# Kernel optimization log

Hardware: AMD Instinct MI355X
Metric: run time of the kernel (lower is better)

## Reference

```python
import jax, jax.numpy as jnp
import numpy as np

KERNEL_SIZE = 5
KERNEL_NUM = 64
STRIDE = 1
PRIOR_VAR = 1.0


def setup_inputs() -> dict:
    key = jax.random.key(0)
    k1, k2 = jax.random.split(key)
    mu_in = jax.random.normal(k1, (128, 128, 128, 3), dtype=jnp.float32)
    # init: normal stddev 0.05 for w_mu, constant -4.6 for w_sigma
    w_mu = 0.05 * jax.random.normal(k2, (KERNEL_SIZE, KERNEL_SIZE, 3, KERNEL_NUM), dtype=jnp.float32)
    w_sigma = jnp.full((KERNEL_NUM,), -4.6, dtype=jnp.float32)
    return {"mu_in": mu_in, "w_mu": w_mu, "w_sigma": w_sigma}


def kl_regularizer_conv(mu, logvar):
    k = mu.shape[-1]
    mu2 = mu.reshape(-1, k)              # [k*k*C, kernel_num]
    n = mu2.shape[0]
    kl = -jnp.mean(1.0 + logvar
                   - jnp.log1p(jnp.exp(logvar)) / PRIOR_VAR
                   - jnp.sum(jnp.square(mu2), axis=0) / (n * PRIOR_VAR))
    kl = jnp.where(jnp.isnan(kl), jnp.float32(1e-05), kl)
    kl = jnp.where(jnp.isinf(kl), jnp.float32(1e-05), kl)
    return kl


def reference(mu_in, w_mu, w_sigma):
    B, H, W, C = mu_in.shape
    ks = KERNEL_SIZE
    kl_conv = kl_regularizer_conv(w_mu, w_sigma)
    w_sigma_2 = jnp.log1p(jnp.exp(w_sigma))  # softplus

    dn = ('NHWC', 'HWIO', 'NHWC')
    mu_out = jax.lax.conv_general_dilated(
        mu_in, w_mu, window_strides=(STRIDE, STRIDE), padding='VALID',
        dimension_numbers=dn)  # [B, Ho, Wo, kernel_num]

    # Per-patch sum of squares == sum-pool conv over squared input summed over C
    # (mathematically identical to extract_patches -> square -> sum, no im2col blowup)
    sq = jnp.sum(jnp.square(mu_in), axis=-1, keepdims=True)  # [B,H,W,1]
    ones_k = jnp.ones((ks, ks, 1, 1), dtype=mu_in.dtype)
    patch_ss = jax.lax.conv_general_dilated(
        sq, ones_k, window_strides=(STRIDE, STRIDE), padding='VALID',
        dimension_numbers=dn)  # [B, Ho, Wo, 1]
    x_dim = jnp.float32(ks * ks * C)
    # broadcast: softplus(w_sigma)[kn] * (sum_sq / x_dim)[B,Ho,Wo,1]
    Sigma_out = w_sigma_2 * (patch_ss / x_dim)  # [B, Ho, Wo, kernel_num]

    Ho = mu_out.shape[1]
    Sigma_out = Sigma_out.reshape(B, Ho, Ho, KERNEL_NUM)
    return (mu_out, Sigma_out, kl_conv)
```

## Files before the change

### kernel.cpp

```cpp
#include <hip/hip_runtime.h>
#include <hip/hip_bf16.h>
#include <math.h>

#define KS 5
#define CIN 3
#define KN 64
#define HIN 128
#define HO 124
#define ROWF (HIN * CIN)
#define NOUT (128LL * 124 * 124 * 64)

typedef short bfrag8 __attribute__((ext_vector_type(8)));
typedef float ffrag4 __attribute__((ext_vector_type(4)));

__device__ __forceinline__ unsigned short f2bf(float f) {
    union { float f; unsigned u; } x;
    x.f = f;
    unsigned r = x.u + 0x7fffu + ((x.u >> 16) & 1u);
    return (unsigned short)(r >> 16);
}

__global__ void kl_kernel(const float* __restrict__ w_mu,
                          const float* __restrict__ w_sigma,
                          float* __restrict__ out_kl) {
    int kn = threadIdx.x;
    float s = 0.f;
#pragma unroll
    for (int i = 0; i < 75; ++i) {
        float m = w_mu[i * KN + kn];
        s = fmaf(m, m, s);
    }
    float lv = w_sigma[kn];
    float sp = log1pf(expf(lv));
    float val = 1.0f + lv - sp - s * (1.0f / 75.0f);
#pragma unroll
    for (int off = 32; off > 0; off >>= 1) val += __shfl_down(val, off);
    if (kn == 0) {
        float kl = -(val / 64.0f);
        if (isnan(kl) || isinf(kl)) kl = 1e-5f;
        out_kl[0] = kl;
    }
}

__global__ __launch_bounds__(256, 4) void conv_kernel(
    const float* __restrict__ mu_in,
    const float* __restrict__ w_mu,
    const float* __restrict__ w_sigma,
    float* __restrict__ mu_out,
    float* __restrict__ sig_out) {

    __shared__ __align__(16) float s_in[2336];
    __shared__ __align__(16) unsigned short s_w[64 * 104];
    __shared__ float s_sp[KN];
    __shared__ float s_cs[HIN];
    __shared__ float s_ssn[HO];

    const int bid = blockIdx.x;
    const int b = bid / HO;
    const int ho = bid % HO;
    const int tid = threadIdx.x;

    const float* src = mu_in + (size_t)(b * HIN + ho) * ROWF;
    for (int i = tid; i < 480; i += 256)
        reinterpret_cast<float4*>(s_in)[i] =
            reinterpret_cast<const float4*>(src)[i];
    for (int i = 1920 + tid; i < 2336; i += 256) s_in[i] = 0.f;

    {
        const int n = tid >> 2;
        const int kbase = (tid & 3) * 26;
#pragma unroll
        for (int kk = 0; kk < 26; ++kk) {
            const int k = kbase + kk;
            float v = 0.f;
            if (k < 80) {
                const int r = k >> 4, t = k & 15;
                if (t < 15) v = w_mu[(r * 15 + t) * KN + n];
            }
            s_w[n * 104 + k] = f2bf(v);
        }
    }
    if (tid < KN) s_sp[tid] = log1pf(expf(w_sigma[tid]));
    __syncthreads();

    if (tid < HIN) {
        float cs = 0.f;
#pragma unroll
        for (int r = 0; r < KS; ++r)
#pragma unroll
            for (int c = 0; c < CIN; ++c) {
                float v = s_in[r * ROWF + tid * CIN + c];
                cs = fmaf(v, v, cs);
            }
        s_cs[tid] = cs;
    }
    __syncthreads();
    if (tid < HO) {
        float ss = s_cs[tid] + s_cs[tid + 1] + s_cs[tid + 2] + s_cs[tid + 3] +
                   s_cs[tid + 4];
        s_ssn[tid] = ss * (1.0f / 75.0f);
    }
    __syncthreads();

    const int lane = tid & 63;
    const int wid = tid >> 6;
    const int lhi = lane >> 4;
    const int llo = lane & 15;

    ffrag4 acc[2][4];
#pragma unroll
    for (int m = 0; m < 2; ++m)
#pragma unroll
        for (int n = 0; n < 4; ++n) acc[m][n] = (ffrag4){0.f, 0.f, 0.f, 0.f};

#pragma unroll
    for (int ks = 0; ks < 3; ++ks) {
        const int k0 = ks * 32 + lhi * 8;
        bfrag8 bfr[4];
#pragma unroll
        for (int nt = 0; nt < 4; ++nt)
            bfr[nt] = *reinterpret_cast<const bfrag8*>(
                &s_w[(nt * 16 + llo) * 104 + k0]);

        const int r = k0 >> 4;
        const int off = k0 & 15;
#pragma unroll
        for (int mt = 0; mt < 2; ++mt) {
            const int wo = wid * 32 + mt * 16 + llo;
            const float* ap = &s_in[r * ROWF + wo * CIN + off];
            bfrag8 afr;
#pragma unroll
            for (int j = 0; j < 8; ++j) afr[j] = (short)f2bf(ap[j]);
#pragma unroll
            for (int nt = 0; nt < 4; ++nt)
                acc[mt][nt] = __builtin_amdgcn_mfma_f32_16x16x32_bf16(
                    afr, bfr[nt], acc[mt][nt], 0, 0, 0);
        }
    }

    float spv[4];
#pragma unroll
    for (int nt = 0; nt < 4; ++nt) spv[nt] = s_sp[nt * 16 + llo];

    const size_t orow = (size_t)(b * HO + ho) * (size_t)(HO * KN);
#pragma unroll
    for (int mt = 0; mt < 2; ++mt) {
#pragma unroll
        for (int rg = 0; rg < 4; ++rg) {
            const int wo = wid * 32 + mt * 16 + lhi * 4 + rg;
            if (wo < HO) {
                const float ssn = s_ssn[wo];
                const size_t obase = orow + (size_t)wo * KN;
#pragma unroll
                for (int nt = 0; nt < 4; ++nt) {
                    const int kn = nt * 16 + llo;
                    mu_out[obase + kn] = acc[mt][nt][rg];
                    sig_out[obase + kn] = spv[nt] * ssn;
                }
            }
        }
    }
}

extern "C" void kernel_launch(void* const* d_in, const int* in_sizes, int n_in,
                              void* d_out, int out_size, void* d_ws,
                              size_t ws_size, hipStream_t stream) {
    const float* mu_in = (const float*)d_in[0];
    const float* w_mu = (const float*)d_in[1];
    const float* w_sigma = (const float*)d_in[2];
    float* out = (float*)d_out;

    float* mu_out = out;
    float* sig_out = out + NOUT;
    float* kl_out = out + 2 * NOUT;

    conv_kernel<<<128 * HO, 256, 0, stream>>>(mu_in, w_mu, w_sigma, mu_out,
                                              sig_out);
    kl_kernel<<<1, 64, 0, stream>>>(w_mu, w_sigma, kl_out);
}
```

Baseline: 265.8 us.

## Precompute bf16 weights once, swap MFMA operands for vectorized float4 output stores

Moves the weight bf16 conversion and softplus into a one-block prep kernel that writes to workspace, so each conv block copies ready weights with vector loads. The input row is pre-converted to bf16 in shared memory once. The MFMA operand roles are swapped (weights as A, input as B) so each lane holds four consecutive output channels and can write mu_out and sig_out with float4 stores instead of scalar stores. This adds a kernel launch and more shared memory, and lowers the occupancy hint from 4 to 3 blocks per CU.

```diff
diff --git a/kernel.cpp b/kernel.cpp
--- a/kernel.cpp
+++ b/kernel.cpp
@@ -9,6 +9,7 @@
 #define HO 124
 #define ROWF (HIN * CIN)
 #define NOUT (128LL * 124 * 124 * 64)
+#define KP 104
 
 typedef short bfrag8 __attribute__((ext_vector_type(8)));
 typedef float ffrag4 __attribute__((ext_vector_type(4)));
@@ -20,6 +21,26 @@
     return (unsigned short)(r >> 16);
 }
 
+__global__ void prep_kernel(const float* __restrict__ w_mu,
+                            const float* __restrict__ w_sigma,
+                            unsigned short* __restrict__ w_bf,
+                            float* __restrict__ sp_out) {
+    const int tid = threadIdx.x;
+    const int n = tid >> 2;
+    const int kbase = (tid & 3) * 26;
+#pragma unroll
+    for (int kk = 0; kk < 26; ++kk) {
+        const int k = kbase + kk;
+        float v = 0.f;
+        if (k < 80) {
+            const int r = k >> 4, t = k & 15;
+            if (t < 15) v = w_mu[(r * 15 + t) * KN + n];
+        }
+        w_bf[n * KP + k] = f2bf(v);
+    }
+    if (tid < KN) sp_out[tid] = log1pf(expf(w_sigma[tid]));
+}
+
 __global__ void kl_kernel(const float* __restrict__ w_mu,
                           const float* __restrict__ w_sigma,
                           float* __restrict__ out_kl) {
@@ -42,18 +63,19 @@
     }
 }
 
-__global__ __launch_bounds__(256, 4) void conv_kernel(
+__global__ __launch_bounds__(256, 3) void conv_kernel(
     const float* __restrict__ mu_in,
-    const float* __restrict__ w_mu,
-    const float* __restrict__ w_sigma,
+    const unsigned short* __restrict__ w_bf,
+    const float* __restrict__ sp_in,
     float* __restrict__ mu_out,
     float* __restrict__ sig_out) {
 
-    __shared__ __align__(16) float s_in[2336];
-    __shared__ __align__(16) unsigned short s_w[64 * 104];
+    __shared__ __align__(16) float s_in[1952];
+    __shared__ __align__(16) unsigned short s_x[128 * KP];
+    __shared__ __align__(16) unsigned short s_w[KN * KP];
     __shared__ float s_sp[KN];
     __shared__ float s_cs[HIN];
-    __shared__ float s_ssn[HO];
+    __shared__ float s_ssn[HIN];
 
     const int bid = blockIdx.x;
     const int b = bid / HO;
@@ -64,23 +86,11 @@
     for (int i = tid; i < 480; i += 256)
         reinterpret_cast<float4*>(s_in)[i] =
             reinterpret_cast<const float4*>(src)[i];
-    for (int i = 1920 + tid; i < 2336; i += 256) s_in[i] = 0.f;
-
-    {
-        const int n = tid >> 2;
-        const int kbase = (tid & 3) * 26;
-#pragma unroll
-        for (int kk = 0; kk < 26; ++kk) {
-            const int k = kbase + kk;
-            float v = 0.f;
-            if (k < 80) {
-                const int r = k >> 4, t = k & 15;
-                if (t < 15) v = w_mu[(r * 15 + t) * KN + n];
-            }
-            s_w[n * 104 + k] = f2bf(v);
-        }
-    }
-    if (tid < KN) s_sp[tid] = log1pf(expf(w_sigma[tid]));
+    if (tid < 32) s_in[1920 + tid] = 0.f;
+    for (int i = tid; i < 832; i += 256)
+        reinterpret_cast<float4*>(s_w)[i] =
+            reinterpret_cast<const float4*>(w_bf)[i];
+    if (tid < KN) s_sp[tid] = sp_in[tid];
     __syncthreads();
 
     if (tid < HIN) {
@@ -95,68 +105,86 @@
         s_cs[tid] = cs;
     }
     __syncthreads();
-    if (tid < HO) {
-        float ss = s_cs[tid] + s_cs[tid + 1] + s_cs[tid + 2] + s_cs[tid + 3] +
-                   s_cs[tid + 4];
-        s_ssn[tid] = ss * (1.0f / 75.0f);
+
+    if (tid < HIN) {
+        float v = 0.f;
+        if (tid < HO)
+            v = (s_cs[tid] + s_cs[tid + 1] + s_cs[tid + 2] + s_cs[tid + 3] +
+                 s_cs[tid + 4]) * (1.0f / 75.0f);
+        s_ssn[tid] = v;
+    }
+    for (int i = tid; i < 640; i += 256) {
+        const int r = i >> 7;
+        const int wo = i & 127;
+        const float* p = &s_in[r * ROWF + wo * CIN];
+        unsigned u[8];
+#pragma unroll
+        for (int j = 0; j < 8; ++j)
+            u[j] = (unsigned)f2bf(p[2 * j]) | ((unsigned)f2bf(p[2 * j + 1]) << 16);
+        uint4* dst = reinterpret_cast<uint4*>(&s_x[wo * KP + r * 16]);
+        dst[0] = make_uint4(u[0], u[1], u[2], u[3]);
+        dst[1] = make_uint4(u[4], u[5], u[6], u[7]);
+    }
+    for (int i = tid; i < 1024; i += 256) {
+        const int wo = i >> 3, j = i & 7;
+        reinterpret_cast<unsigned*>(s_x)[wo * (KP / 2) + 40 + j] = 0u;
     }
     __syncthreads();
 
     const int lane = tid & 63;
     const int wid = tid >> 6;
+    const int llo = lane & 15;
     const int lhi = lane >> 4;
-    const int llo = lane & 15;
+
+    bfrag8 afr[4][3];
+#pragma unroll
+    for (int mt = 0; mt < 4; ++mt)
+#pragma unroll
+        for (int ks = 0; ks < 3; ++ks)
+            afr[mt][ks] = *reinterpret_cast<const bfrag8*>(
+                &s_w[(mt * 16 + llo) * KP + ks * 32 + lhi * 8]);
 
     ffrag4 acc[2][4];
 #pragma unroll
-    for (int m = 0; m < 2; ++m)
-#pragma unroll
-        for (int n = 0; n < 4; ++n) acc[m][n] = (ffrag4){0.f, 0.f, 0.f, 0.f};
-
-#pragma unroll
-    for (int ks = 0; ks < 3; ++ks) {
-        const int k0 = ks * 32 + lhi * 8;
-        bfrag8 bfr[4];
-#pragma unroll
-        for (int nt = 0; nt < 4; ++nt)
-            bfr[nt] = *reinterpret_cast<const bfrag8*>(
-                &s_w[(nt * 16 + llo) * 104 + k0]);
-
-        const int r = k0 >> 4;
-        const int off = k0 & 15;
-#pragma unroll
-        for (int mt = 0; mt < 2; ++mt) {
-            const int wo = wid * 32 + mt * 16 + llo;
-            const float* ap = &s_in[r * ROWF + wo * CIN + off];
-            bfrag8 afr;
-#pragma unroll
-            for (int j = 0; j < 8; ++j) afr[j] = (short)f2bf(ap[j]);
-#pragma unroll
-            for (int nt = 0; nt < 4; ++nt)
-                acc[mt][nt] = __builtin_amdgcn_mfma_f32_16x16x32_bf16(
-                    afr, bfr[nt], acc[mt][nt], 0, 0, 0);
+    for (int nt = 0; nt < 2; ++nt)
+#pragma unroll
+        for (int mt = 0; mt < 4; ++mt) acc[nt][mt] = (ffrag4){0.f, 0.f, 0.f, 0.f};
+
+#pragma unroll
+    for (int nt = 0; nt < 2; ++nt) {
+        const int wo = (wid * 2 + nt) * 16 + llo;
+#pragma unroll
+        for (int ks = 0; ks < 3; ++ks) {
+            bfrag8 bfr = *reinterpret_cast<const bfrag8*>(
+                &s_x[wo * KP + ks * 32 + lhi * 8]);
+#pragma unroll
+            for (int mt = 0; mt < 4; ++mt)
+                acc[nt][mt] = __builtin_amdgcn_mfma_f32_16x16x32_bf16(
+                    afr[mt][ks], bfr, acc[nt][mt], 0, 0, 0);
         }
     }
 
-    float spv[4];
-#pragma unroll
-    for (int nt = 0; nt < 4; ++nt) spv[nt] = s_sp[nt * 16 + llo];
+    float4 sp4[4];
+#pragma unroll
+    for (int mt = 0; mt < 4; ++mt)
+        sp4[mt] = *reinterpret_cast<const float4*>(&s_sp[mt * 16 + lhi * 4]);
 
     const size_t orow = (size_t)(b * HO + ho) * (size_t)(HO * KN);
 #pragma unroll
-    for (int mt = 0; mt < 2; ++mt) {
-#pragma unroll
-        for (int rg = 0; rg < 4; ++rg) {
-            const int wo = wid * 32 + mt * 16 + lhi * 4 + rg;
-            if (wo < HO) {
-                const float ssn = s_ssn[wo];
-                const size_t obase = orow + (size_t)wo * KN;
-#pragma unroll
-                for (int nt = 0; nt < 4; ++nt) {
-                    const int kn = nt * 16 + llo;
-                    mu_out[obase + kn] = acc[mt][nt][rg];
-                    sig_out[obase + kn] = spv[nt] * ssn;
-                }
+    for (int nt = 0; nt < 2; ++nt) {
+        const int wo = (wid * 2 + nt) * 16 + llo;
+        if (wo < HO) {
+            const float ssn = s_ssn[wo];
+            const size_t obase = orow + (size_t)wo * KN;
+#pragma unroll
+            for (int mt = 0; mt < 4; ++mt) {
+                const int knb = mt * 16 + lhi * 4;
+                *reinterpret_cast<float4*>(&mu_out[obase + knb]) =
+                    make_float4(acc[nt][mt][0], acc[nt][mt][1], acc[nt][mt][2],
+                                acc[nt][mt][3]);
+                *reinterpret_cast<float4*>(&sig_out[obase + knb]) =
+                    make_float4(sp4[mt].x * ssn, sp4[mt].y * ssn,
+                                sp4[mt].z * ssn, sp4[mt].w * ssn);
             }
         }
     }
@@ -174,7 +202,11 @@
     float* sig_out = out + NOUT;
     float* kl_out = out + 2 * NOUT;
 
-    conv_kernel<<<128 * HO, 256, 0, stream>>>(mu_in, w_mu, w_sigma, mu_out,
+    unsigned short* w_bf = (unsigned short*)d_ws;
+    float* sp_ws = (float*)((char*)d_ws + KN * KP * 2);
+
+    prep_kernel<<<1, 256, 0, stream>>>(w_mu, w_sigma, w_bf, sp_ws);
+    conv_kernel<<<128 * HO, 256, 0, stream>>>(mu_in, w_bf, sp_ws, mu_out,
                                               sig_out);
     kl_kernel<<<1, 64, 0, stream>>>(w_mu, w_sigma, kl_out);
 }
```

Measured after the change: 248.0 us. -6.7%, faster.
